# Performance work log

Measured on AMD Instinct MI355X. Metric: run time of the kernel, lower is better.

## Reference

```python
import jax, jax.numpy as jnp
import numpy as np

VAT_TOKENS = 57
ACTION_NUM = 56
NUM_HEADS = 16
DIM = 1152
HEAD_DIM = DIM // NUM_HEADS
SCALE = HEAD_DIM ** -0.5
N_GROUPS = 3  # num_non_act = 768 -> 3 groups of 256


def setup_inputs() -> dict:
    key = jax.random.key(0)
    ks = jax.random.split(key, 8)
    B, N, C = 32, VAT_TOKENS + 768, DIM
    w_std = C ** -0.5
    return {
        "x": jax.random.normal(ks[0], (B, N, C), jnp.float32),
        "w_qkv_non": jax.random.normal(ks[1], (3 * C, C), jnp.float32) * w_std,
        "w_q_act": jax.random.normal(ks[2], (C, C), jnp.float32) * w_std,
        "w_kv_act": jax.random.normal(ks[3], (2 * C, C), jnp.float32) * w_std,
        "w_proj_non": jax.random.normal(ks[4], (C, C), jnp.float32) * w_std,
        "b_proj_non": jnp.zeros((C,), jnp.float32),
        "w_proj_act": jax.random.normal(ks[5], (C, C), jnp.float32) * w_std,
        "b_proj_act": jnp.zeros((C,), jnp.float32),
    }


def reference(x, w_qkv_non, w_q_act, w_kv_act, w_proj_non, b_proj_non,
              w_proj_act, b_proj_act):
    B, N, C = x.shape
    H, Dh = NUM_HEADS, HEAD_DIM
    num_non_act = N - VAT_TOKENS
    G = num_non_act // N_GROUPS  # group size (256)

    # ---- non-action stream: windowed (grouped) self-attention ----
    non_act = x[:, VAT_TOKENS:]                                  # (B, 768, C)
    qkv = non_act @ w_qkv_non.T                                  # (B, 768, 3C)
    qkv = qkv.reshape(B, N_GROUPS, G, 3, H, Dh)
    q = qkv[:, :, :, 0]                                          # (B, g, G, H, Dh)
    k = qkv[:, :, :, 1]
    v = qkv[:, :, :, 2]
    attn = jnp.einsum('bgqhd,bgkhd->bghqk', q, k) * SCALE
    attn = jax.nn.softmax(attn, axis=-1)
    x_non = jnp.einsum('bghqk,bgkhd->bgqhd', attn, v)
    x_non = x_non.reshape(B, num_non_act, C)

    # ---- action stream: act queries attend to x[ACTION_NUM:] ----
    act = x[:, :VAT_TOKENS]
    q_act = (act @ w_q_act.T).reshape(B, VAT_TOKENS, H, Dh)
    kv = (x @ w_kv_act.T).reshape(B, N, 2, H, Dh)
    k_act = kv[:, ACTION_NUM:, 0]                                # (B, N-56, H, Dh)
    v_act = kv[:, ACTION_NUM:, 1]
    attn_act = jnp.einsum('bqhd,bkhd->bhqk', q_act, k_act) * SCALE
    attn_act = jax.nn.softmax(attn_act, axis=-1)
    x_act = jnp.einsum('bhqk,bkhd->bqhd', attn_act, v_act)
    x_act = x_act.reshape(B, VAT_TOKENS, C)

    # ---- output projections + concat ----
    x_non = x_non @ w_proj_non.T + b_proj_non
    x_act = x_act @ w_proj_act.T + b_proj_act
    return jnp.concatenate([x_act, x_non], axis=1)
```

## Files before the change

kernel.cpp:

```cpp
#include <hip/hip_runtime.h>

typedef __attribute__((ext_vector_type(8))) __bf16 bf16x8;
typedef __attribute__((ext_vector_type(4))) float f32x4;
typedef __attribute__((ext_vector_type(4))) unsigned short u16x4;
typedef __attribute__((ext_vector_type(8))) unsigned short u16x8;

#define MFMA_BF16 __builtin_amdgcn_mfma_f32_16x16x32_bf16

__device__ __forceinline__ unsigned short f2bf(float f) {
  union { float f; unsigned u; } v; v.f = f;
  unsigned r = v.u + 0x7FFFu + ((v.u >> 16) & 1u);
  return (unsigned short)(r >> 16);
}

__device__ __forceinline__ void gload16(const void* g, void* l) {
  __builtin_amdgcn_global_load_lds(
      (const __attribute__((address_space(1))) unsigned int*)g,
      (__attribute__((address_space(3))) unsigned int*)l, 16, 0, 0);
}

__global__ void __launch_bounds__(256) cast_bf16_kernel(const float* __restrict__ in,
                                                        unsigned short* __restrict__ out,
                                                        int n8) {
  int i = blockIdx.x * 256 + threadIdx.x;
  if (i >= n8) return;
  long base = (long)i * 8;
  float4 a = *(const float4*)(in + base);
  float4 b = *(const float4*)(in + base + 4);
  u16x8 o;
  o[0] = f2bf(a.x); o[1] = f2bf(a.y); o[2] = f2bf(a.z); o[3] = f2bf(a.w);
  o[4] = f2bf(b.x); o[5] = f2bf(b.y); o[6] = f2bf(b.z); o[7] = f2bf(b.w);
  *(u16x8*)(out + base) = o;
}

template <int REMAP>
__device__ __forceinline__ long remap_row(int m) {
  if (REMAP == 1) { int b = m / 768; return (long)b * 825 + 57 + (m - b * 768); }
  if (REMAP == 2) { int b = m / 57;  return (long)b * 825 + (m - b * 57); }
  return m;
}

template <int REMAP, bool PROJ>
__global__ void __launch_bounds__(512, 2) gemm256(const unsigned short* __restrict__ A,
                                                  const unsigned short* __restrict__ Bw,
                                                  void* __restrict__ Cout,
                                                  const float* __restrict__ bias,
                                                  int M, int N) {
  const int K = 1152;
  const int NT = 18;
  __shared__ unsigned short L[65536];
  unsigned short* Al = L;
  unsigned short* Bl = L + 32768;
  int tid = threadIdx.x;
  int lane = tid & 63;
  int wid = tid >> 6;
  int l15 = lane & 15, hi = lane >> 4;
  int wm = wid >> 2, wn = wid & 3;

  int gx = gridDim.x;
  int nwg = gx * gridDim.y;
  int orig = blockIdx.y * gx + blockIdx.x;
  int q8 = nwg >> 3, r8 = nwg & 7;
  int xcd = orig & 7, off = orig >> 3;
  int wgid = (xcd < r8 ? xcd * (q8 + 1) : r8 * (q8 + 1) + (xcd - r8) * q8) + off;
  int bn = wgid % gx, bm = wgid / gx;
  int m0 = bm * 256, n0 = bn * 256;

  int rlo = tid >> 2;
  int cg = ((tid & 3) - (tid >> 3)) & 3;
  int ma0 = m0 + rlo;       if (ma0 > M - 1) ma0 = M - 1;
  int ma1 = m0 + rlo + 128; if (ma1 > M - 1) ma1 = M - 1;
  const unsigned short* aptr0 = A + remap_row<REMAP>(ma0) * K + cg * 8;
  const unsigned short* aptr1 = A + remap_row<REMAP>(ma1) * K + cg * 8;
  int nb0 = n0 + rlo;       if (nb0 > N - 1) nb0 = N - 1;
  int nb1 = n0 + rlo + 128; if (nb1 > N - 1) nb1 = N - 1;
  const unsigned short* bptr0 = Bw + (long)nb0 * K + cg * 8;
  const unsigned short* bptr1 = Bw + (long)nb1 * K + cg * 8;
  unsigned ldst = (unsigned)tid * 8;

  unsigned short* Ad = Al + ldst;
  unsigned short* Bd = Bl + ldst;

  const int cl = (hi + (l15 >> 1)) & 3;
  const unsigned short* arb[4];
  const unsigned short* brb[4];
#pragma unroll
  for (int f = 0; f < 4; ++f) {
    arb[f] = Al + (wm * 128 + f * 16 + l15) * 32 + cl * 8;
    brb[f] = Bl + (wn * 64 + f * 16 + l15) * 32 + cl * 8;
  }

#define STAGE_A(tt, hh)                                                        \
  {                                                                            \
    gload16(aptr0 + ((tt) * 64 + (hh) * 32), Ad + ((((2 * (tt) + (hh)) & 3)) << 13)); \
    gload16(aptr1 + ((tt) * 64 + (hh) * 32), Ad + ((((2 * (tt) + (hh)) & 3)) << 13) + 4096); \
  }
#define STAGE_B(tt, hh)                                                        \
  {                                                                            \
    gload16(bptr0 + ((tt) * 64 + (hh) * 32), Bd + ((((2 * (tt) + (hh)) & 3)) << 13)); \
    gload16(bptr1 + ((tt) * 64 + (hh) * 32), Bd + ((((2 * (tt) + (hh)) & 3)) << 13) + 4096); \
  }

  STAGE_A(0, 0); STAGE_B(0, 0); STAGE_A(0, 1); STAGE_B(0, 1);
  __builtin_amdgcn_sched_barrier(0);
  asm volatile("s_waitcnt vmcnt(4)" ::: "memory");
  __builtin_amdgcn_s_barrier();
  __builtin_amdgcn_sched_barrier(0);

  f32x4 acc[8][4] = {};

#pragma unroll
  for (int t = 0; t < NT; ++t) {
#pragma unroll
    for (int h = 0; h < 2; ++h) {
      const int slot = (2 * t + h) & 3;
      const int roff = slot << 13;
      bf16x8 af[8];
#pragma unroll
      for (int f = 0; f < 8; ++f)
        af[f] = *(const bf16x8*)(arb[f & 3] + roff + (f >> 2) * 2048);
      bf16x8 bfr[4];
#pragma unroll
      for (int f = 0; f < 4; ++f) bfr[f] = *(const bf16x8*)(brb[f] + roff);
      if (t + 1 < NT) { STAGE_A(t + 1, h); STAGE_B(t + 1, h); }
      __builtin_amdgcn_s_setprio(1);
#pragma unroll
      for (int fm = 0; fm < 8; ++fm)
#pragma unroll
        for (int fn = 0; fn < 4; ++fn)
          acc[fm][fn] = MFMA_BF16(af[fm], bfr[fn], acc[fm][fn], 0, 0, 0);
      __builtin_amdgcn_s_setprio(0);
      if (t + 1 < NT) asm volatile("s_waitcnt vmcnt(4)" ::: "memory");
      else            asm volatile("s_waitcnt vmcnt(0)" ::: "memory");
      __builtin_amdgcn_sched_barrier(0);
      __builtin_amdgcn_s_barrier();
      __builtin_amdgcn_sched_barrier(0);
    }
  }
#undef STAGE_A
#undef STAGE_B

  if (!PROJ) {
    unsigned short* reg = L + wid * 8192;
#pragma unroll
    for (int a = 0; a < 8; ++a) {
#pragma unroll
      for (int fn = 0; fn < 4; ++fn) {
        int rbase = a * 16 + hi * 4;
#pragma unroll
        for (int r = 0; r < 4; ++r) {
          int row = rbase + r;
          int ch = (fn * 2 + (l15 >> 3)) ^ (row & 7);
          reg[row * 64 + ch * 8 + (l15 & 7)] = f2bf(acc[a][fn][r]);
        }
      }
    }
#pragma unroll
    for (int i = 0; i < 16; ++i) {
      int rr = i * 8 + (lane >> 3);
      int ch = (lane & 7) ^ (rr & 7);
      u16x8 v = *(const u16x8*)(reg + rr * 64 + ch * 8);
      int m = m0 + wm * 128 + rr;
      int n = n0 + wn * 64 + (lane & 7) * 8;
      if (m < M && n < N)
        *(u16x8*)((unsigned short*)Cout + (long)m * N + n) = v;
    }
  } else {
    float* regf = (float*)L + wid * 4096;
    float bv[4];
#pragma unroll
    for (int fn = 0; fn < 4; ++fn) {
      int n = n0 + wn * 64 + fn * 16 + l15;
      bv[fn] = bias[n < N ? n : N - 1];
    }
#pragma unroll
    for (int half = 0; half < 2; ++half) {
#pragma unroll
      for (int a4 = 0; a4 < 4; ++a4) {
#pragma unroll
        for (int fn = 0; fn < 4; ++fn) {
          int rbase = a4 * 16 + hi * 4;
#pragma unroll
          for (int r = 0; r < 4; ++r)
            regf[(rbase + r) * 64 + fn * 16 + l15] = acc[half * 4 + a4][fn][r] + bv[fn];
        }
      }
#pragma unroll
      for (int i = 0; i < 16; ++i) {
        int rr = i * 4 + (lane >> 4);
        int cc = (lane & 15) * 4;
        f32x4 v = *(const f32x4*)(regf + rr * 64 + cc);
        int m = m0 + wm * 128 + half * 64 + rr;
        int n = n0 + wn * 64 + cc;
        if (m < M && n < N)
          *(f32x4*)((float*)Cout + remap_row<REMAP>(m) * N + n) = v;
      }
      if (half == 0) asm volatile("s_waitcnt lgkmcnt(0)" ::: "memory");
    }
  }
}

template <int REMAP, bool PROJ>
__global__ void __launch_bounds__(256) gemm_bt(const unsigned short* __restrict__ A,
                                               const unsigned short* __restrict__ Bw,
                                               void* __restrict__ Cout,
                                               const float* __restrict__ bias,
                                               int M, int N) {
  const int K = 1152;
  __shared__ unsigned short At[128 * 64];
  __shared__ unsigned short Bt[128 * 64];
  int tid = threadIdx.x;
  int lane = tid & 63, wid = tid >> 6;
  int l15 = lane & 15, hi = lane >> 4;
  int wm = wid >> 1, wn = wid & 1;
  int m0 = blockIdx.y * 128, n0 = blockIdx.x * 128;

  const unsigned short* asrc[4];
  const unsigned short* bsrc[4];
  unsigned ldsoff[4];
#pragma unroll
  for (int j = 0; j < 4; j++) {
    int c = tid + j * 256;
    int r = c >> 3;
    int cc = (c & 7) ^ (r & 7);
    ldsoff[j] = (unsigned)c * 8;
    int ma = m0 + r; if (ma > M - 1) ma = M - 1;
    asrc[j] = A + remap_row<REMAP>(ma) * K + cc * 8;
    bsrc[j] = Bw + (long)(n0 + r) * K + cc * 8;
  }

  f32x4 acc[4][4] = {};

  for (int kt = 0; kt < K; kt += 64) {
#pragma unroll
    for (int j = 0; j < 4; j++) {
      gload16(asrc[j] + kt, &At[ldsoff[j]]);
      gload16(bsrc[j] + kt, &Bt[ldsoff[j]]);
    }
    __syncthreads();
#pragma unroll
    for (int ks = 0; ks < 2; ks++) {
      bf16x8 af[4], bfr[4];
#pragma unroll
      for (int i = 0; i < 4; i++) {
        int ra = wm * 64 + i * 16 + l15;
        int ca = (ks * 64 + hi * 16) ^ ((ra & 7) << 4);
        af[i] = *(const bf16x8*)((const char*)At + ra * 128 + ca);
        int rb = wn * 64 + i * 16 + l15;
        int cb = (ks * 64 + hi * 16) ^ ((rb & 7) << 4);
        bfr[i] = *(const bf16x8*)((const char*)Bt + rb * 128 + cb);
      }
#pragma unroll
      for (int i = 0; i < 4; i++)
#pragma unroll
        for (int j = 0; j < 4; j++)
          acc[i][j] = MFMA_BF16(af[i], bfr[j], acc[i][j], 0, 0, 0);
    }
    __syncthreads();
  }

#pragma unroll
  for (int j = 0; j < 4; j++) {
    int n = n0 + wn * 64 + j * 16 + l15;
    float bv = 0.f;
    if (PROJ) bv = bias[n];
#pragma unroll
    for (int i = 0; i < 4; i++) {
      int mb = m0 + wm * 64 + i * 16 + hi * 4;
#pragma unroll
      for (int r = 0; r < 4; r++) {
        int m = mb + r;
        if (m < M) {
          if (PROJ)
            ((float*)Cout)[remap_row<REMAP>(m) * N + n] = acc[i][j][r] + bv;
          else
            ((unsigned short*)Cout)[(long)m * N + n] = f2bf(acc[i][j][r]);
        }
      }
    }
  }
}

__global__ void __launch_bounds__(256) attn_non(const unsigned short* __restrict__ qkv,
                                                unsigned short* __restrict__ o) {
  int h = blockIdx.x, g = blockIdx.y, b = blockIdx.z;
  __shared__ unsigned short K_s[128 * 104];
  __shared__ unsigned short V_s[80 * 136];
  __shared__ unsigned short P_s[16 * 16 * 40];
  int tid = threadIdx.x, lane = tid & 63, wid = tid >> 6;
  int l15 = lane & 15, hi = lane >> 4;
  const long base = (long)((b * 3 + g) * 256) * 3456;
  const float SC2 = 0.11785113019775793f * 1.4426950408889634f;

  bf16x8 qf[4][3];
#pragma unroll
  for (int qt = 0; qt < 4; qt++)
#pragma unroll
    for (int ds = 0; ds < 3; ds++) {
      int q = wid * 64 + qt * 16 + l15;
      int d = ds * 32 + hi * 8;
      if (d < 72)
        qf[qt][ds] = *(const bf16x8*)(qkv + base + (long)q * 3456 + h * 72 + d);
      else {
        u16x8 z = {0, 0, 0, 0, 0, 0, 0, 0};
        qf[qt][ds] = __builtin_bit_cast(bf16x8, z);
      }
    }

  f32x4 ot[5][4] = {};
  float lsum[4] = {0.f, 0.f, 0.f, 0.f};

  for (int c0 = 0; c0 < 256; c0 += 128) {
    {
      int r = tid >> 1, hf = tid & 1;
      const unsigned short* src = qkv + base + (long)(c0 + r) * 3456 + (16 + h) * 72 + hf * 48;
      unsigned short* dst = &K_s[r * 104 + hf * 48];
#pragma unroll
      for (int j = 0; j < 6; j++) {
        int col = hf * 48 + j * 8;
        u16x8 v = {0, 0, 0, 0, 0, 0, 0, 0};
        if (col < 72) v = *(const u16x8*)(src + j * 8);
        *(u16x8*)(dst + j * 8) = v;
      }
    }
    if (tid < 128) {
      const unsigned short* src = qkv + base + (long)(c0 + tid) * 3456 + (32 + h) * 72;
      u16x8 w[9];
#pragma unroll
      for (int j = 0; j < 9; j++) w[j] = *(const u16x8*)(src + j * 8);
#pragma unroll
      for (int j = 0; j < 9; j++)
#pragma unroll
        for (int e = 0; e < 8; e++) V_s[(j * 8 + e) * 136 + tid] = w[j][e];
    }
    __syncthreads();

#pragma unroll
    for (int k32 = 0; k32 < 4; k32++) {
#pragma unroll
      for (int kt = 0; kt < 2; kt++) {
        bf16x8 kf[3];
#pragma unroll
        for (int ds = 0; ds < 3; ds++)
          kf[ds] = *(const bf16x8*)((const char*)K_s +
                     ((k32 * 32 + kt * 16 + l15) * 104 + ds * 32 + hi * 8) * 2);
#pragma unroll
        for (int qt = 0; qt < 4; qt++) {
          f32x4 st = {};
#pragma unroll
          for (int ds = 0; ds < 3; ds++) st = MFMA_BF16(kf[ds], qf[qt][ds], st, 0, 0, 0);
          u16x4 pw;
#pragma unroll
          for (int r = 0; r < 4; r++) {
            float p = exp2f(st[r] * SC2);
            lsum[qt] += p;
            pw[r] = f2bf(p);
          }
          *(u16x4*)&P_s[((wid * 4 + qt) * 16 + l15) * 40 + kt * 16 + hi * 4] = pw;
        }
      }
      bf16x8 pf[4];
#pragma unroll
      for (int qt = 0; qt < 4; qt++)
        pf[qt] = *(const bf16x8*)&P_s[((wid * 4 + qt) * 16 + l15) * 40 + hi * 8];
#pragma unroll
      for (int dt = 0; dt < 5; dt++) {
        bf16x8 vf = *(const bf16x8*)&V_s[(dt * 16 + l15) * 136 + k32 * 32 + hi * 8];
#pragma unroll
        for (int qt = 0; qt < 4; qt++) ot[dt][qt] = MFMA_BF16(vf, pf[qt], ot[dt][qt], 0, 0, 0);
      }
    }
    __syncthreads();
  }

#pragma unroll
  for (int qt = 0; qt < 4; qt++) {
    float s = lsum[qt];
    s += __shfl_xor(s, 16);
    s += __shfl_xor(s, 32);
    lsum[qt] = 1.0f / s;
  }
#pragma unroll
  for (int dt = 0; dt < 5; dt++)
#pragma unroll
    for (int qt = 0; qt < 4; qt++)
#pragma unroll
      for (int r = 0; r < 4; r++) {
        int d = dt * 16 + hi * 4 + r;
        if (d < 72) {
          long row = (long)b * 825 + 57 + g * 256 + wid * 64 + qt * 16 + l15;
          o[row * 1152 + h * 72 + d] = f2bf(ot[dt][qt][r] * lsum[qt]);
        }
      }
}

__global__ void __launch_bounds__(256) attn_act(const unsigned short* __restrict__ kv,
                                                const unsigned short* __restrict__ qa,
                                                unsigned short* __restrict__ o) {
  int h = blockIdx.x, b = blockIdx.y;
  __shared__ unsigned short K_s[128 * 104];
  __shared__ unsigned short V_s[80 * 136];
  __shared__ unsigned short P_s[4 * 16 * 40];
  int tid = threadIdx.x, lane = tid & 63, wid = tid >> 6;
  int l15 = lane & 15, hi = lane >> 4;
  const float SC2 = 0.11785113019775793f * 1.4426950408889634f;
  const int LIM = 769;

  bf16x8 qf[3];
  {
    int q = wid * 16 + l15; if (q > 56) q = 56;
#pragma unroll
    for (int ds = 0; ds < 3; ds++) {
      int d = ds * 32 + hi * 8;
      if (d < 72)
        qf[ds] = *(const bf16x8*)(qa + (long)(b * 57 + q) * 1152 + h * 72 + d);
      else {
        u16x8 z = {0, 0, 0, 0, 0, 0, 0, 0};
        qf[ds] = __builtin_bit_cast(bf16x8, z);
      }
    }
  }

  f32x4 ot[5] = {};
  float lsum = 0.f;
  const long kbase = (long)b * 825 + 56;

  for (int c0 = 0; c0 < LIM; c0 += 128) {
    int valid = LIM - c0; if (valid > 128) valid = 128;
    {
      int r = tid >> 1, hf = tid & 1;
      int rr = r < valid ? r : valid - 1;
      const unsigned short* src = kv + (kbase + c0 + rr) * 2304 + h * 72 + hf * 48;
      unsigned short* dst = &K_s[r * 104 + hf * 48];
#pragma unroll
      for (int j = 0; j < 6; j++) {
        int col = hf * 48 + j * 8;
        u16x8 v = {0, 0, 0, 0, 0, 0, 0, 0};
        if (col < 72) v = *(const u16x8*)(src + j * 8);
        *(u16x8*)(dst + j * 8) = v;
      }
    }
    if (tid < 128) {
      int rr = tid < valid ? tid : valid - 1;
      const unsigned short* src = kv + (kbase + c0 + rr) * 2304 + (16 + h) * 72;
      u16x8 w[9];
#pragma unroll
      for (int j = 0; j < 9; j++) w[j] = *(const u16x8*)(src + j * 8);
#pragma unroll
      for (int j = 0; j < 9; j++)
#pragma unroll
        for (int e = 0; e < 8; e++) V_s[(j * 8 + e) * 136 + tid] = w[j][e];
    }
    __syncthreads();

#pragma unroll
    for (int k32 = 0; k32 < 4; k32++) {
#pragma unroll
      for (int kt = 0; kt < 2; kt++) {
        bf16x8 kf[3];
#pragma unroll
        for (int ds = 0; ds < 3; ds++)
          kf[ds] = *(const bf16x8*)((const char*)K_s +
                     ((k32 * 32 + kt * 16 + l15) * 104 + ds * 32 + hi * 8) * 2);
        f32x4 st = {};
#pragma unroll
        for (int ds = 0; ds < 3; ds++) st = MFMA_BF16(kf[ds], qf[ds], st, 0, 0, 0);
        u16x4 pw;
#pragma unroll
        for (int r = 0; r < 4; r++) {
          int kg = c0 + k32 * 32 + kt * 16 + hi * 4 + r;
          float p = (kg < LIM) ? exp2f(st[r] * SC2) : 0.f;
          lsum += p;
          pw[r] = f2bf(p);
        }
        *(u16x4*)&P_s[(wid * 16 + l15) * 40 + kt * 16 + hi * 4] = pw;
      }
      bf16x8 pf = *(const bf16x8*)&P_s[(wid * 16 + l15) * 40 + hi * 8];
#pragma unroll
      for (int dt = 0; dt < 5; dt++) {
        bf16x8 vf = *(const bf16x8*)&V_s[(dt * 16 + l15) * 136 + k32 * 32 + hi * 8];
        ot[dt] = MFMA_BF16(vf, pf, ot[dt], 0, 0, 0);
      }
    }
    __syncthreads();
  }

  {
    float s = lsum;
    s += __shfl_xor(s, 16);
    s += __shfl_xor(s, 32);
    lsum = 1.0f / s;
  }
  int q = wid * 16 + l15;
#pragma unroll
  for (int dt = 0; dt < 5; dt++)
#pragma unroll
    for (int r = 0; r < 4; r++) {
      int d = dt * 16 + hi * 4 + r;
      if (d < 72 && q < 57)
        o[((long)b * 825 + q) * 1152 + h * 72 + d] = f2bf(ot[dt][r] * lsum);
    }
}

extern "C" void kernel_launch(void* const* d_in, const int* in_sizes, int n_in,
                              void* d_out, int out_size, void* d_ws, size_t ws_size,
                              hipStream_t stream) {
  const float* x     = (const float*)d_in[0];
  const float* w_qkv = (const float*)d_in[1];
  const float* w_q   = (const float*)d_in[2];
  const float* w_kv  = (const float*)d_in[3];
  const float* w_pn  = (const float*)d_in[4];
  const float* b_pn  = (const float*)d_in[5];
  const float* w_pa  = (const float*)d_in[6];
  const float* b_pa  = (const float*)d_in[7];

  char* ws = (char*)d_ws;
  unsigned short* xb    = (unsigned short*)ws; ws += (size_t)26400 * 1152 * 2;
  unsigned short* wqkvb = (unsigned short*)ws; ws += (size_t)3456 * 1152 * 2;
  unsigned short* wqb   = (unsigned short*)ws; ws += (size_t)1152 * 1152 * 2;
  unsigned short* wkvb  = (unsigned short*)ws; ws += (size_t)2304 * 1152 * 2;
  unsigned short* wpnb  = (unsigned short*)ws; ws += (size_t)1152 * 1152 * 2;
  unsigned short* wpab  = (unsigned short*)ws; ws += (size_t)1152 * 1152 * 2;
  unsigned short* qkvw  = (unsigned short*)ws; ws += (size_t)24576 * 3456 * 2;
  unsigned short* kvw   = (unsigned short*)ws; ws += (size_t)26400 * 2304 * 2;
  unsigned short* qw    = (unsigned short*)ws; ws += (size_t)1824 * 1152 * 2;
  unsigned short* attnw = (unsigned short*)ws; ws += (size_t)26400 * 1152 * 2;

  auto cast = [&](const float* src, unsigned short* dst, long n) {
    int n8 = (int)(n / 8);
    cast_bf16_kernel<<<(n8 + 255) / 256, 256, 0, stream>>>(src, dst, n8);
  };
  cast(x,     xb,    26400L * 1152);
  cast(w_qkv, wqkvb, 3456L * 1152);
  cast(w_q,   wqb,   1152L * 1152);
  cast(w_kv,  wkvb,  2304L * 1152);
  cast(w_pn,  wpnb,  1152L * 1152);
  cast(w_pa,  wpab,  1152L * 1152);

  gemm256<1, false><<<dim3(14, 96), 512, 0, stream>>>(xb, wqkvb, qkvw, nullptr, 24576, 3456);
  gemm256<0, false><<<dim3(9, 104), 512, 0, stream>>>(xb, wkvb, kvw, nullptr, 26400, 2304);
  gemm_bt<2, false><<<dim3(9, 15), 256, 0, stream>>>(xb, wqb, qw, nullptr, 1824, 1152);

  attn_non<<<dim3(16, 3, 32), 256, 0, stream>>>(qkvw, attnw);
  attn_act<<<dim3(16, 32), 256, 0, stream>>>(kvw, qw, attnw);

  gemm256<1, true><<<dim3(5, 96), 512, 0, stream>>>(attnw, wpnb, d_out, b_pn, 24576, 1152);
  gemm_bt<2, true><<<dim3(9, 15), 256, 0, stream>>>(attnw, wpab, d_out, b_pa, 1824, 1152);
}
```

Before: 741.5 us.

## Retile big GEMMs to 256x192 with 12 waves and register double-buffered fragments

Replaces the 256x256, 8-wave GEMM with a 256x192 tile run by 12 waves of 64x64 each. K-steps are now 32 wide with a 4-slot LDS ring staged three steps ahead, and A fragments are double-buffered in registers across steps. The N dimensions 3456, 2304 and 1152 divide evenly by 192, so edge tiles that were partly wasted with 256-wide tiles go away, and each wave holds fewer accumulators. The cost is more barriers per K step, lower arithmetic intensity per tile, and higher register pressure from the 768-thread launch bound.

```diff
diff --git a/kernel.cpp b/kernel.cpp
--- a/kernel.cpp
+++ b/kernel.cpp
@@ -41,21 +41,19 @@
 }
 
 template <int REMAP, bool PROJ>
-__global__ void __launch_bounds__(512, 2) gemm256(const unsigned short* __restrict__ A,
-                                                  const unsigned short* __restrict__ Bw,
-                                                  void* __restrict__ Cout,
-                                                  const float* __restrict__ bias,
-                                                  int M, int N) {
+__global__ void __launch_bounds__(768, 3) gemm256b(const unsigned short* __restrict__ A,
+                                                   const unsigned short* __restrict__ Bw,
+                                                   void* __restrict__ Cout,
+                                                   const float* __restrict__ bias,
+                                                   int M, int N) {
   const int K = 1152;
-  const int NT = 18;
-  __shared__ unsigned short L[65536];
+  __shared__ unsigned short L[57344];
   unsigned short* Al = L;
   unsigned short* Bl = L + 32768;
   int tid = threadIdx.x;
-  int lane = tid & 63;
-  int wid = tid >> 6;
+  int lane = tid & 63, wid = tid >> 6;
   int l15 = lane & 15, hi = lane >> 4;
-  int wm = wid >> 2, wn = wid & 3;
+  int wm = wid & 3, wn = wid >> 2;
 
   int gx = gridDim.x;
   int nwg = gx * gridDim.y;
@@ -64,86 +62,84 @@
   int xcd = orig & 7, off = orig >> 3;
   int wgid = (xcd < r8 ? xcd * (q8 + 1) : r8 * (q8 + 1) + (xcd - r8) * q8) + off;
   int bn = wgid % gx, bm = wgid / gx;
-  int m0 = bm * 256, n0 = bn * 256;
-
-  int rlo = tid >> 2;
-  int cg = ((tid & 3) - (tid >> 3)) & 3;
-  int ma0 = m0 + rlo;       if (ma0 > M - 1) ma0 = M - 1;
-  int ma1 = m0 + rlo + 128; if (ma1 > M - 1) ma1 = M - 1;
-  const unsigned short* aptr0 = A + remap_row<REMAP>(ma0) * K + cg * 8;
-  const unsigned short* aptr1 = A + remap_row<REMAP>(ma1) * K + cg * 8;
-  int nb0 = n0 + rlo;       if (nb0 > N - 1) nb0 = N - 1;
-  int nb1 = n0 + rlo + 128; if (nb1 > N - 1) nb1 = N - 1;
-  const unsigned short* bptr0 = Bw + (long)nb0 * K + cg * 8;
-  const unsigned short* bptr1 = Bw + (long)nb1 * K + cg * 8;
-  unsigned ldst = (unsigned)tid * 8;
-
-  unsigned short* Ad = Al + ldst;
-  unsigned short* Bd = Bl + ldst;
+  int m0 = bm * 256, n0 = bn * 192;
+
+  int c1 = tid;
+  int c2 = 768 + (tid & 255);
+  int r1 = c1 >> 2, r2 = c2 >> 2;
+  int cg1 = ((c1 & 3) - (c1 >> 3)) & 3;
+  int cg2 = ((c2 & 3) - (c2 >> 3)) & 3;
+  int ma1 = m0 + r1; if (ma1 > M - 1) ma1 = M - 1;
+  int ma2 = m0 + r2; if (ma2 > M - 1) ma2 = M - 1;
+  const unsigned short* aP1 = A + remap_row<REMAP>(ma1) * K + cg1 * 8;
+  const unsigned short* aP2 = A + remap_row<REMAP>(ma2) * K + cg2 * 8;
+  int nb1 = n0 + r1; if (nb1 > N - 1) nb1 = N - 1;
+  const unsigned short* bP = Bw + (long)nb1 * K + cg1 * 8;
+  unsigned short* AdA = Al + c1 * 8;
+  unsigned short* AdB = Al + c2 * 8;
+  unsigned short* BdA = Bl + c1 * 8;
 
   const int cl = (hi + (l15 >> 1)) & 3;
-  const unsigned short* arb[4];
-  const unsigned short* brb[4];
-#pragma unroll
-  for (int f = 0; f < 4; ++f) {
-    arb[f] = Al + (wm * 128 + f * 16 + l15) * 32 + cl * 8;
-    brb[f] = Bl + (wn * 64 + f * 16 + l15) * 32 + cl * 8;
-  }
-
-#define STAGE_A(tt, hh)                                                        \
-  {                                                                            \
-    gload16(aptr0 + ((tt) * 64 + (hh) * 32), Ad + ((((2 * (tt) + (hh)) & 3)) << 13)); \
-    gload16(aptr1 + ((tt) * 64 + (hh) * 32), Ad + ((((2 * (tt) + (hh)) & 3)) << 13) + 4096); \
-  }
-#define STAGE_B(tt, hh)                                                        \
-  {                                                                            \
-    gload16(bptr0 + ((tt) * 64 + (hh) * 32), Bd + ((((2 * (tt) + (hh)) & 3)) << 13)); \
-    gload16(bptr1 + ((tt) * 64 + (hh) * 32), Bd + ((((2 * (tt) + (hh)) & 3)) << 13) + 4096); \
-  }
-
-  STAGE_A(0, 0); STAGE_B(0, 0); STAGE_A(0, 1); STAGE_B(0, 1);
+  const unsigned short* arR = Al + (wm * 64 + l15) * 32 + cl * 8;
+  const unsigned short* brR = Bl + (wn * 64 + l15) * 32 + cl * 8;
+
+#define STAGE(P)                                                   \
+  {                                                                \
+    gload16(aP1 + (P) * 32, AdA + (((P) & 3) << 13));              \
+    gload16(aP2 + (P) * 32, AdB + (((P) & 3) << 13));              \
+    gload16(bP + (P) * 32, BdA + (((P) & 3) * 6144));              \
+  }
+#define READ_FA(P, S)                                              \
+  {                                                                \
+    _Pragma("unroll") for (int f = 0; f < 4; ++f)                  \
+        fA[S][f] = *(const bf16x8*)(arR + (((P) & 3) * 8192) + f * 512); \
+  }
+#define READ_FB(P)                                                 \
+  {                                                                \
+    _Pragma("unroll") for (int f = 0; f < 4; ++f)                  \
+        fB[f] = *(const bf16x8*)(brR + (((P) & 3) * 6144) + f * 512);   \
+  }
+
+  STAGE(0); STAGE(1); STAGE(2);
   __builtin_amdgcn_sched_barrier(0);
-  asm volatile("s_waitcnt vmcnt(4)" ::: "memory");
+  asm volatile("s_waitcnt vmcnt(3)" ::: "memory");
   __builtin_amdgcn_s_barrier();
   __builtin_amdgcn_sched_barrier(0);
 
-  f32x4 acc[8][4] = {};
-
-#pragma unroll
-  for (int t = 0; t < NT; ++t) {
-#pragma unroll
-    for (int h = 0; h < 2; ++h) {
-      const int slot = (2 * t + h) & 3;
-      const int roff = slot << 13;
-      bf16x8 af[8];
-#pragma unroll
-      for (int f = 0; f < 8; ++f)
-        af[f] = *(const bf16x8*)(arb[f & 3] + roff + (f >> 2) * 2048);
-      bf16x8 bfr[4];
-#pragma unroll
-      for (int f = 0; f < 4; ++f) bfr[f] = *(const bf16x8*)(brb[f] + roff);
-      if (t + 1 < NT) { STAGE_A(t + 1, h); STAGE_B(t + 1, h); }
-      __builtin_amdgcn_s_setprio(1);
-#pragma unroll
-      for (int fm = 0; fm < 8; ++fm)
-#pragma unroll
-        for (int fn = 0; fn < 4; ++fn)
-          acc[fm][fn] = MFMA_BF16(af[fm], bfr[fn], acc[fm][fn], 0, 0, 0);
-      __builtin_amdgcn_s_setprio(0);
-      if (t + 1 < NT) asm volatile("s_waitcnt vmcnt(4)" ::: "memory");
-      else            asm volatile("s_waitcnt vmcnt(0)" ::: "memory");
+  bf16x8 fA[2][4];
+  bf16x8 fB[4];
+  READ_FA(0, 0);
+  READ_FB(0);
+  f32x4 acc[4][4] = {};
+
+#pragma unroll
+  for (int p = 0; p < 36; ++p) {
+    if (p < 35) READ_FA(p + 1, (p + 1) & 1);
+    __builtin_amdgcn_s_setprio(1);
+#pragma unroll
+    for (int a = 0; a < 4; ++a)
+#pragma unroll
+      for (int fn = 0; fn < 4; ++fn)
+        acc[a][fn] = MFMA_BF16(fA[p & 1][a], fB[fn], acc[a][fn], 0, 0, 0);
+    __builtin_amdgcn_s_setprio(0);
+    if (p < 35) READ_FB(p + 1);
+    if (p <= 32) STAGE(p + 3);
+    if (p <= 32)      asm volatile("s_waitcnt vmcnt(3)" ::: "memory");
+    else if (p <= 34) asm volatile("s_waitcnt vmcnt(0)" ::: "memory");
+    if (p < 35) {
       __builtin_amdgcn_sched_barrier(0);
       __builtin_amdgcn_s_barrier();
       __builtin_amdgcn_sched_barrier(0);
     }
   }
-#undef STAGE_A
-#undef STAGE_B
+#undef STAGE
+#undef READ_FA
+#undef READ_FB
 
   if (!PROJ) {
-    unsigned short* reg = L + wid * 8192;
-#pragma unroll
-    for (int a = 0; a < 8; ++a) {
+    unsigned short* reg = L + wid * 4096;
+#pragma unroll
+    for (int a = 0; a < 4; ++a) {
 #pragma unroll
       for (int fn = 0; fn < 4; ++fn) {
         int rbase = a * 16 + hi * 4;
@@ -156,17 +152,17 @@
       }
     }
 #pragma unroll
-    for (int i = 0; i < 16; ++i) {
+    for (int i = 0; i < 8; ++i) {
       int rr = i * 8 + (lane >> 3);
       int ch = (lane & 7) ^ (rr & 7);
       u16x8 v = *(const u16x8*)(reg + rr * 64 + ch * 8);
-      int m = m0 + wm * 128 + rr;
+      int m = m0 + wm * 64 + rr;
       int n = n0 + wn * 64 + (lane & 7) * 8;
       if (m < M && n < N)
         *(u16x8*)((unsigned short*)Cout + (long)m * N + n) = v;
     }
   } else {
-    float* regf = (float*)L + wid * 4096;
+    float* regf = (float*)L + wid * 2048;
     float bv[4];
 #pragma unroll
     for (int fn = 0; fn < 4; ++fn) {
@@ -176,21 +172,21 @@
 #pragma unroll
     for (int half = 0; half < 2; ++half) {
 #pragma unroll
-      for (int a4 = 0; a4 < 4; ++a4) {
+      for (int a2 = 0; a2 < 2; ++a2) {
 #pragma unroll
         for (int fn = 0; fn < 4; ++fn) {
-          int rbase = a4 * 16 + hi * 4;
+          int rbase = a2 * 16 + hi * 4;
 #pragma unroll
           for (int r = 0; r < 4; ++r)
-            regf[(rbase + r) * 64 + fn * 16 + l15] = acc[half * 4 + a4][fn][r] + bv[fn];
+            regf[(rbase + r) * 64 + fn * 16 + l15] = acc[half * 2 + a2][fn][r] + bv[fn];
         }
       }
 #pragma unroll
-      for (int i = 0; i < 16; ++i) {
+      for (int i = 0; i < 8; ++i) {
         int rr = i * 4 + (lane >> 4);
         int cc = (lane & 15) * 4;
         f32x4 v = *(const f32x4*)(regf + rr * 64 + cc);
-        int m = m0 + wm * 128 + half * 64 + rr;
+        int m = m0 + wm * 64 + half * 32 + rr;
         int n = n0 + wn * 64 + cc;
         if (m < M && n < N)
           *(f32x4*)((float*)Cout + remap_row<REMAP>(m) * N + n) = v;
@@ -537,13 +533,13 @@
   cast(w_pn,  wpnb,  1152L * 1152);
   cast(w_pa,  wpab,  1152L * 1152);
 
-  gemm256<1, false><<<dim3(14, 96), 512, 0, stream>>>(xb, wqkvb, qkvw, nullptr, 24576, 3456);
-  gemm256<0, false><<<dim3(9, 104), 512, 0, stream>>>(xb, wkvb, kvw, nullptr, 26400, 2304);
+  gemm256b<1, false><<<dim3(18, 96), 768, 0, stream>>>(xb, wqkvb, qkvw, nullptr, 24576, 3456);
+  gemm256b<0, false><<<dim3(12, 104), 768, 0, stream>>>(xb, wkvb, kvw, nullptr, 26400, 2304);
   gemm_bt<2, false><<<dim3(9, 15), 256, 0, stream>>>(xb, wqb, qw, nullptr, 1824, 1152);
 
   attn_non<<<dim3(16, 3, 32), 256, 0, stream>>>(qkvw, attnw);
   attn_act<<<dim3(16, 32), 256, 0, stream>>>(kvw, qw, attnw);
 
-  gemm256<1, true><<<dim3(5, 96), 512, 0, stream>>>(attnw, wpnb, d_out, b_pn, 24576, 1152);
+  gemm256b<1, true><<<dim3(6, 96), 768, 0, stream>>>(attnw, wpnb, d_out, b_pn, 24576, 1152);
   gemm_bt<2, true><<<dim3(9, 15), 256, 0, stream>>>(attnw, wpab, d_out, b_pa, 1824, 1152);
 }
```

After: 783.7 us. 1.06x slower.

## Deepen GEMM LDS prefetch to three stages and double-buffer A fragments

Applied to the files above, without the earlier changes.

Reworks the gemm256 main loop into 36 half-K phases. Global-to-LDS loads now run three phases ahead across the four LDS slots, instead of one. The A fragments for the next phase are read from LDS into a second register buffer before the MFMA block, and the B fragments are read after it. This is meant to hide global-load and LDS-read latency behind MFMA work. The cost is more live vector registers at 2 waves per SIMD, which could cause spills, and more complex wait and barrier ordering.

```diff
diff --git a/kernel.cpp b/kernel.cpp
--- a/kernel.cpp
+++ b/kernel.cpp
@@ -47,7 +47,6 @@
                                                   const float* __restrict__ bias,
                                                   int M, int N) {
   const int K = 1152;
-  const int NT = 18;
   __shared__ unsigned short L[65536];
   unsigned short* Al = L;
   unsigned short* Bl = L + 32768;
@@ -90,55 +89,61 @@
     brb[f] = Bl + (wn * 64 + f * 16 + l15) * 32 + cl * 8;
   }
 
-#define STAGE_A(tt, hh)                                                        \
-  {                                                                            \
-    gload16(aptr0 + ((tt) * 64 + (hh) * 32), Ad + ((((2 * (tt) + (hh)) & 3)) << 13)); \
-    gload16(aptr1 + ((tt) * 64 + (hh) * 32), Ad + ((((2 * (tt) + (hh)) & 3)) << 13) + 4096); \
-  }
-#define STAGE_B(tt, hh)                                                        \
-  {                                                                            \
-    gload16(bptr0 + ((tt) * 64 + (hh) * 32), Bd + ((((2 * (tt) + (hh)) & 3)) << 13)); \
-    gload16(bptr1 + ((tt) * 64 + (hh) * 32), Bd + ((((2 * (tt) + (hh)) & 3)) << 13) + 4096); \
-  }
-
-  STAGE_A(0, 0); STAGE_B(0, 0); STAGE_A(0, 1); STAGE_B(0, 1);
+#define STAGE(P)                                                        \
+  {                                                                     \
+    gload16(aptr0 + (P) * 32, Ad + (((P) & 3) << 13));                  \
+    gload16(aptr1 + (P) * 32, Ad + ((((P) & 3) << 13)) + 4096);         \
+    gload16(bptr0 + (P) * 32, Bd + (((P) & 3) << 13));                  \
+    gload16(bptr1 + (P) * 32, Bd + ((((P) & 3) << 13)) + 4096);         \
+  }
+#define READ_FA(P, S)                                                   \
+  {                                                                     \
+    _Pragma("unroll") for (int f = 0; f < 8; ++f)                       \
+        fA[S][f] = *(const bf16x8*)(arb[f & 3] + (((P) & 3) << 13) + (f >> 2) * 2048); \
+  }
+#define READ_FB(P)                                                      \
+  {                                                                     \
+    _Pragma("unroll") for (int f = 0; f < 4; ++f)                       \
+        fB[f] = *(const bf16x8*)(brb[f] + (((P) & 3) << 13));           \
+  }
+
+  STAGE(0); STAGE(1); STAGE(2);
   __builtin_amdgcn_sched_barrier(0);
   asm volatile("s_waitcnt vmcnt(4)" ::: "memory");
   __builtin_amdgcn_s_barrier();
   __builtin_amdgcn_sched_barrier(0);
 
+  bf16x8 fA[2][8];
+  bf16x8 fB[4];
+  READ_FA(0, 0);
+  READ_FB(0);
   f32x4 acc[8][4] = {};
 
 #pragma unroll
-  for (int t = 0; t < NT; ++t) {
-#pragma unroll
-    for (int h = 0; h < 2; ++h) {
-      const int slot = (2 * t + h) & 3;
-      const int roff = slot << 13;
-      bf16x8 af[8];
-#pragma unroll
-      for (int f = 0; f < 8; ++f)
-        af[f] = *(const bf16x8*)(arb[f & 3] + roff + (f >> 2) * 2048);
-      bf16x8 bfr[4];
-#pragma unroll
-      for (int f = 0; f < 4; ++f) bfr[f] = *(const bf16x8*)(brb[f] + roff);
-      if (t + 1 < NT) { STAGE_A(t + 1, h); STAGE_B(t + 1, h); }
-      __builtin_amdgcn_s_setprio(1);
-#pragma unroll
-      for (int fm = 0; fm < 8; ++fm)
-#pragma unroll
-        for (int fn = 0; fn < 4; ++fn)
-          acc[fm][fn] = MFMA_BF16(af[fm], bfr[fn], acc[fm][fn], 0, 0, 0);
-      __builtin_amdgcn_s_setprio(0);
-      if (t + 1 < NT) asm volatile("s_waitcnt vmcnt(4)" ::: "memory");
-      else            asm volatile("s_waitcnt vmcnt(0)" ::: "memory");
+  for (int p = 0; p < 36; ++p) {
+    const int cur = p & 1;
+    if (p < 35) READ_FA(p + 1, cur ^ 1);
+    __builtin_amdgcn_sched_barrier(0);
+    __builtin_amdgcn_s_setprio(1);
+#pragma unroll
+    for (int fm = 0; fm < 8; ++fm)
+#pragma unroll
+      for (int fn = 0; fn < 4; ++fn)
+        acc[fm][fn] = MFMA_BF16(fA[cur][fm], fB[fn], acc[fm][fn], 0, 0, 0);
+    __builtin_amdgcn_s_setprio(0);
+    if (p < 35) READ_FB(p + 1);
+    if (p <= 32) STAGE(p + 3);
+    if (p <= 32)      asm volatile("s_waitcnt vmcnt(4)" ::: "memory");
+    else if (p == 33) asm volatile("s_waitcnt vmcnt(0)" ::: "memory");
+    if (p < 35) {
       __builtin_amdgcn_sched_barrier(0);
       __builtin_amdgcn_s_barrier();
       __builtin_amdgcn_sched_barrier(0);
     }
   }
-#undef STAGE_A
-#undef STAGE_B
+#undef STAGE
+#undef READ_FA
+#undef READ_FB
 
   if (!PROJ) {
     unsigned short* reg = L + wid * 8192;
```

New measurement: 737.0 us. Within noise of the previous version (-0.6%).
